# Kernel optimization log

Measured on AMD Instinct MI355X. Metric: run time of the kernel, lower is better.

## Reference

```python
import jax, jax.numpy as jnp
import numpy as np

B, T = 64, 512
V, E, H, O = 50000, 300, 256, 512
NUM_LAYERS = 2


def setup_inputs() -> dict:
    key = jax.random.key(0)
    ks = jax.random.split(key, 24)
    def p(k, shape, s=0.05):
        return jax.random.normal(k, shape, dtype=jnp.float32) * s
    inp = {"text": jax.random.randint(ks[0], (B, T), 0, V)}
    inp["emb"] = p(ks[1], (V, E), 0.1)
    in_dims = [E, 2 * H]  # layer0 sees embeddings, layer1 sees bidir concat
    idx = 2
    for l in range(NUM_LAYERS):
        for d in ("f", "b"):
            inp[f"l{l}{d}_Wih"] = p(ks[idx], (4 * H, in_dims[l])); idx += 1
            inp[f"l{l}{d}_Whh"] = p(ks[idx], (4 * H, H)); idx += 1
            inp[f"l{l}{d}_bih"] = p(ks[idx], (4 * H,)); idx += 1
            inp[f"l{l}{d}_bhh"] = p(ks[idx], (4 * H,)); idx += 1
    inp["fc_W"] = p(ks[idx], (O, 2 * H))
    inp["fc_b"] = p(ks[idx + 1], (O,))
    return inp


def lstm_dir(x, Wih, Whh, bih, bhh, reverse):
    """Single-direction LSTM. x: [B,T,in]. Returns (outputs [B,T,H], h_n [B,H]).
    PyTorch gate order: input, forget, cell(g), output."""
    Bsz = x.shape[0]
    Hd = Whh.shape[1]
    # Precompute input contribution for all timesteps (one big GEMM).
    xg = jnp.einsum('bti,gi->btg', x, Wih) + bih  # [B,T,4H]
    xg = jnp.swapaxes(xg, 0, 1)                    # [T,B,4H]

    def step(carry, xg_t):
        h, c = carry
        gates = xg_t + h @ Whh.T + bhh
        i, f, g, o = jnp.split(gates, 4, axis=-1)
        c = jax.nn.sigmoid(f) * c + jax.nn.sigmoid(i) * jnp.tanh(g)
        h = jax.nn.sigmoid(o) * jnp.tanh(c)
        return (h, c), h

    init = (jnp.zeros((Bsz, Hd), x.dtype), jnp.zeros((Bsz, Hd), x.dtype))
    (h_n, _), ys = jax.lax.scan(step, init, xg, reverse=reverse)
    return jnp.swapaxes(ys, 0, 1), h_n


def reference(text, emb,
              l0f_Wih, l0f_Whh, l0f_bih, l0f_bhh,
              l0b_Wih, l0b_Whh, l0b_bih, l0b_bhh,
              l1f_Wih, l1f_Whh, l1f_bih, l1f_bhh,
              l1b_Wih, l1b_Whh, l1b_bih, l1b_bhh,
              fc_W, fc_b):
    x = emb[text]  # [B,T,E] embedding lookup
    # Layer 0 (bidirectional)
    yf, _ = lstm_dir(x, l0f_Wih, l0f_Whh, l0f_bih, l0f_bhh, False)
    yb, _ = lstm_dir(x, l0b_Wih, l0b_Whh, l0b_bih, l0b_bhh, True)
    x1 = jnp.concatenate([yf, yb], axis=-1)  # [B,T,2H]
    # Layer 1 (bidirectional); only final hidden states are needed
    _, hf = lstm_dir(x1, l1f_Wih, l1f_Whh, l1f_bih, l1f_bhh, False)
    _, hb = lstm_dir(x1, l1b_Wih, l1b_Whh, l1b_bih, l1b_bhh, True)
    hidden = jnp.concatenate([hf, hb], axis=-1)  # [B,2H] == hidden[-2]++hidden[-1]
    # dropout is identity in eval mode
    return hidden @ fc_W.T + fc_b  # [B,O]
```

## Files before the change

kernel.cpp:

```cpp
#include <hip/hip_runtime.h>

typedef unsigned short u16;
typedef __attribute__((ext_vector_type(4))) float f32x4;
typedef __attribute__((ext_vector_type(8))) __bf16 bf16x8;
typedef __attribute__((ext_vector_type(4))) u16 u16x4;

#define TSEQ 512
#define BATCH 64
#define HDIM 256
#define KD   512
#define GDIM 1024
#define EDIM 300
#define ELDA 304
#define TC   128
#define NC   4

__device__ __forceinline__ float b2f(u16 u){
  union { unsigned int i; float f; } v; v.i = ((unsigned int)u) << 16; return v.f;
}
__device__ __forceinline__ u16 f2b(float f){
  union { float f; unsigned int i; } v; v.f = f;
  unsigned int x = v.i;
  unsigned int r = (x + 0x7fffu + ((x >> 16) & 1u)) >> 16;
  return (u16)r;
}
__device__ __forceinline__ float sigm(float x){
  return __builtin_amdgcn_rcpf(1.f + __expf(-x));
}
__device__ __forceinline__ float tanh_(float x){
  float e = __expf(2.f * x);
  return 1.f - 2.f * __builtin_amdgcn_rcpf(e + 1.f);
}
__device__ __forceinline__ f32x4 mfma16(bf16x8 a, bf16x8 b, f32x4 c){
  return __builtin_amdgcn_mfma_f32_16x16x32_bf16(a, b, c, 0, 0, 0);
}

struct Cvt6 {
  const float* src[4];
  u16* dst[4];
  int cum[5];
};
__global__ void k6_cvt(Cvt6 a){
  int g = blockIdx.x * 256 + threadIdx.x;
  if (g >= a.cum[4]) return;
  int s = 0;
#pragma unroll
  for (int i = 1; i < 4; ++i) if (g >= a.cum[i]) s = i;
  int off = g - a.cum[s];
  f32x4 v = *(const f32x4*)(a.src[s] + (size_t)off * 4);
  u16x4 o = { f2b(v[0]), f2b(v[1]), f2b(v[2]), f2b(v[3]) };
  *(u16x4*)(a.dst[s] + (size_t)off * 4) = o;
}

struct CvtW6 { const float* src[4]; u16* dst; };
__global__ void k6_cvtw(CvtW6 a){
  int g = blockIdx.x * 256 + threadIdx.x;
  int mat = g >> 16;
  int rem = g & 65535;
  int row = rem >> 6, c4 = rem & 63;
  f32x4 v = *(const f32x4*)(a.src[mat] + (size_t)row * HDIM + c4 * 4);
  u16x4 hi = { f2b(v[0]), f2b(v[1]), f2b(v[2]), f2b(v[3]) };
  f32x4 r = { v[0] - b2f(hi[0]), v[1] - b2f(hi[1]), v[2] - b2f(hi[2]), v[3] - b2f(hi[3]) };
  u16x4 lo = { f2b(r[0]), f2b(r[1]), f2b(r[2]), f2b(r[3]) };
  u16* base = a.dst + (size_t)mat * GDIM * KD + (size_t)row * KD;
  *(u16x4*)(base + c4 * 4) = hi;
  *(u16x4*)(base + HDIM + c4 * 4) = lo;
}

struct Bias6 { const float* a[4]; const float* b[4]; float* d[4]; };
__global__ void k6_bias(Bias6 z){
  int k = blockIdx.x, i = threadIdx.x;
  z.d[k][i] = z.a[k][i] + z.b[k][i];
}

__global__ void k6_embed(const int* __restrict__ text, const float* __restrict__ emb,
                         u16* __restrict__ xbf){
  int row = blockIdx.x;
  int t = threadIdx.x;
  if (t >= 75) return;
  int tok = text[row];
  f32x4 v = *(const f32x4*)(emb + (size_t)tok * EDIM + t * 4);
  u16x4 o = { f2b(v[0]), f2b(v[1]), f2b(v[2]), f2b(v[3]) };
  *(u16x4*)(xbf + (size_t)row * ELDA + t * 4) = o;
}

struct Gemm6 {
  const u16* A; long lda; int K, KT;
  const u16* W0; const u16* W1; long ldw;
  const float* bias0; const float* bias1;
  float* out;
  int tb0, tb1;
};
__global__ __launch_bounds__(256, 2) void k6_gemm(Gemm6 g){
  const int bm = blockIdx.x, bn = blockIdx.y, z = blockIdx.z;
  const u16* W = z ? g.W1 : g.W0;
  const float* bias = z ? g.bias1 : g.bias0;
  const int tbase = z ? g.tb1 : g.tb0;
  float* outp = g.out + (size_t)z * BATCH * TC * GDIM;
  const int tid = threadIdx.x;
  const int l = tid & 63, l15 = l & 15, lq = l >> 4;
  const int wid = tid >> 6, wm = wid >> 1, wn = wid & 1;

  __shared__ u16 At[2][128 * 40];
  __shared__ u16 Bt[2][128 * 40];

  f32x4 acc[4][4];
#pragma unroll
  for (int i = 0; i < 4; ++i)
#pragma unroll
    for (int j = 0; j < 4; ++j) acc[i][j] = (f32x4){0.f, 0.f, 0.f, 0.f};

  u16x4 alo[2], ahi[2], blo[2], bhi[2];

  auto LOAD = [&](int kt){
#pragma unroll
    for (int c = 0; c < 2; ++c){
      int idx = c * 256 + tid;
      int row = idx >> 2, seg = idx & 3;
      int k0 = kt * 32 + seg * 8;
      int gm = bm * 128 + row;
      size_t arow = (size_t)(gm >> 7) * TSEQ + tbase + (gm & 127);
      if (k0 + 8 <= g.K){
        const u16* p = g.A + arow * g.lda + k0;
        alo[c] = *(const u16x4*)p; ahi[c] = *(const u16x4*)(p + 4);
      } else {
        u16 tmp[8];
#pragma unroll
        for (int e = 0; e < 8; ++e){
          int k = k0 + e;
          tmp[e] = (k < g.K) ? g.A[arow * g.lda + k] : (u16)0;
        }
        alo[c] = (u16x4){tmp[0], tmp[1], tmp[2], tmp[3]};
        ahi[c] = (u16x4){tmp[4], tmp[5], tmp[6], tmp[7]};
      }
      int gn = bn * 128 + row;
      if (k0 + 8 <= g.K){
        const u16* p = W + (size_t)gn * g.ldw + k0;
        blo[c] = *(const u16x4*)p; bhi[c] = *(const u16x4*)(p + 4);
      } else {
        u16 tmp[8];
#pragma unroll
        for (int e = 0; e < 8; ++e){
          int k = k0 + e;
          tmp[e] = (k < g.K) ? W[(size_t)gn * g.ldw + k] : (u16)0;
        }
        blo[c] = (u16x4){tmp[0], tmp[1], tmp[2], tmp[3]};
        bhi[c] = (u16x4){tmp[4], tmp[5], tmp[6], tmp[7]};
      }
    }
  };
  auto STORE = [&](int buf){
#pragma unroll
    for (int c = 0; c < 2; ++c){
      int idx = c * 256 + tid;
      int row = idx >> 2, seg = idx & 3;
      *(u16x4*)&At[buf][row * 40 + seg * 8] = alo[c];
      *(u16x4*)&At[buf][row * 40 + seg * 8 + 4] = ahi[c];
      *(u16x4*)&Bt[buf][row * 40 + seg * 8] = blo[c];
      *(u16x4*)&Bt[buf][row * 40 + seg * 8 + 4] = bhi[c];
    }
  };

  LOAD(0); STORE(0); __syncthreads();
  for (int kt = 0; kt < g.KT; ++kt){
    int cur = kt & 1;
    bool more = (kt + 1 < g.KT);
    if (more) LOAD(kt + 1);
    bf16x8 a[4], b[4];
#pragma unroll
    for (int mi = 0; mi < 4; ++mi)
      a[mi] = *(const bf16x8*)&At[cur][(wm * 64 + mi * 16 + l15) * 40 + lq * 8];
#pragma unroll
    for (int ni = 0; ni < 4; ++ni)
      b[ni] = *(const bf16x8*)&Bt[cur][(wn * 64 + ni * 16 + l15) * 40 + lq * 8];
#pragma unroll
    for (int mi = 0; mi < 4; ++mi)
#pragma unroll
      for (int ni = 0; ni < 4; ++ni)
        acc[mi][ni] = mfma16(a[mi], b[ni], acc[mi][ni]);
    if (more) STORE(cur ^ 1);
    __syncthreads();
  }

#pragma unroll
  for (int mi = 0; mi < 4; ++mi){
#pragma unroll
    for (int ni = 0; ni < 4; ++ni){
      int gn = bn * 128 + wn * 64 + ni * 16 + l15;
      float bs = bias[gn];
#pragma unroll
      for (int r = 0; r < 4; ++r){
        int gm = bm * 128 + wm * 64 + mi * 16 + lq * 4 + r;
        outp[(size_t)gm * GDIM + gn] = acc[mi][ni][r] + bs;
      }
    }
  }
}

__global__ __launch_bounds__(512, 2)
void k6_rec(const float* __restrict__ xgc,
            const u16* __restrict__ whhL,
            u16* __restrict__ y,
            float* __restrict__ hid,
            float* __restrict__ stc, float* __restrict__ stef, u16* __restrict__ sth,
            int tb0, int tb1, int first, int write_y, int write_hid)
{
  const int dir = blockIdx.x & 1;
  const int b0  = (blockIdx.x >> 1) << 4;
  const int tid = threadIdx.x;
  const int w   = tid >> 6;
  const int l   = tid & 63;
  const int l15 = l & 15;
  const int lq  = l >> 4;
  const int rev = dir;

  __shared__ u16 hbuf[16 * 256];
  __shared__ u16 ws1[8 * 16 * KD];

  const u16* whhd = whhL + (size_t)dir * GDIM * KD;

  int tn16[8];
#pragma unroll
  for (int s = 0; s < 8; ++s) tn16[s] = ((s >> 1) * 16 + 2 * w + (s & 1)) * 16;

  {
    const int tb = tn16[0];
    char* wreg = (char*)ws1 + w * 16384;
#pragma unroll
    for (int r = 0; r < 16; ++r){
      bf16x8 v = *(const bf16x8*)(whhd + (size_t)(tb + r) * KD + l * 8);
      *(bf16x8*)(wreg + r * 1024 + ((l * 16) ^ ((r & 7) << 4))) = v;
    }
  }

  const u16* sb[7];
#pragma unroll
  for (int ss = 0; ss < 7; ++ss)
    sb[ss] = whhd + (size_t)(tn16[1 + ss] + l15) * KD + lq * 8;

  int koff[8];
#pragma unroll
  for (int kc = 0; kc < 8; ++kc) koff[kc] = (kc * 64 + lq * 16) ^ ((l15 & 7) << 4);
  const int aoff = l15 * 512;
  const char* hbp = (const char*)hbuf;
  const char* wsp = (const char*)ws1 + w * 16384 + l15 * 1024;

  float cst[8], ef[8], hregf[8];
  u16 hreg[8];

  if (first){
    *(f32x4*)((char*)hbuf + tid * 16) = (f32x4){0.f, 0.f, 0.f, 0.f};
#pragma unroll
    for (int i = 0; i < 8; ++i){ cst[i] = 0.f; ef[i] = 0.f; hregf[i] = 0.f; hreg[i] = 0; }
  } else {
#pragma unroll
    for (int th = 0; th < 2; ++th)
#pragma unroll
      for (int r = 0; r < 4; ++r){
        const int idx = th * 4 + r;
        const int m = lq * 4 + r;
        const int j = 32 * w + th * 16 + l15;
        const size_t si = ((size_t)(dir * BATCH + b0 + m)) * HDIM + j;
        cst[idx] = stc[si]; ef[idx] = stef[si];
        u16 hv = sth[si]; hreg[idx] = hv; hregf[idx] = 0.f;
        *(u16*)((char*)hbuf + m * 512 + ((2 * j) ^ ((m & 7) << 4))) = hv;
      }
  }

  size_t xrow[4];
  const int tt0 = rev ? (TC - 1) : 0;
#pragma unroll
  for (int r = 0; r < 4; ++r)
    xrow[r] = ((size_t)dir * BATCH + b0 + lq * 4 + r) * (size_t)(TC * GDIM)
            + (size_t)tt0 * GDIM + l15;
  const long xstep = rev ? -(long)GDIM : (long)GDIM;

#pragma unroll 1
  for (int t = 0; t < TC; ++t){
    const int te = rev ? (tb1 + TC - 1 - t) : (tb0 + t);
    __syncthreads();

    float xgv[8][4];
#pragma unroll
    for (int s = 0; s < 8; ++s)
#pragma unroll
      for (int r = 0; r < 4; ++r) xgv[s][r] = xgc[xrow[r] + tn16[s]];

    f32x4 acc[8];
#pragma unroll
    for (int s = 0; s < 8; ++s) acc[s] = (f32x4){0.f, 0.f, 0.f, 0.f};

    bf16x8 rb[2][7];
#pragma unroll
    for (int pk = 0; pk < 2; ++pk)
#pragma unroll
      for (int ss = 0; ss < 7; ++ss) rb[pk][ss] = *(const bf16x8*)(sb[ss] + pk * 32);

#pragma unroll
    for (int kc = 0; kc < 16; ++kc){
      bf16x8 af = *(const bf16x8*)(hbp + aoff + koff[kc & 7]);
      bf16x8 w0 = *(const bf16x8*)(wsp + ((kc * 64 + lq * 16) ^ ((l15 & 7) << 4)));
      bf16x8 c1 = rb[kc & 1][0], c2 = rb[kc & 1][1], c3 = rb[kc & 1][2];
      bf16x8 c4 = rb[kc & 1][3], c5 = rb[kc & 1][4], c6 = rb[kc & 1][5], c7 = rb[kc & 1][6];
      if (kc + 2 < 16){
#pragma unroll
        for (int ss = 0; ss < 7; ++ss)
          rb[kc & 1][ss] = *(const bf16x8*)(sb[ss] + (kc + 2) * 32);
      }
      acc[0] = mfma16(af, w0, acc[0]);
      acc[1] = mfma16(af, c1, acc[1]);
      acc[2] = mfma16(af, c2, acc[2]);
      acc[3] = mfma16(af, c3, acc[3]);
      acc[4] = mfma16(af, c4, acc[4]);
      acc[5] = mfma16(af, c5, acc[5]);
      acc[6] = mfma16(af, c6, acc[6]);
      acc[7] = mfma16(af, c7, acc[7]);
    }

    __syncthreads();

#pragma unroll
    for (int th = 0; th < 2; ++th){
#pragma unroll
      for (int r = 0; r < 4; ++r){
        const int idx = th * 4 + r;
        float gi = acc[0 + th][r] + xgv[0 + th][r];
        float gf = acc[2 + th][r] + xgv[2 + th][r];
        float gg = acc[4 + th][r] + xgv[4 + th][r];
        float go = acc[6 + th][r] + xgv[6 + th][r];
        float c = sigm(gf) * cst[idx] + sigm(gi) * tanh_(gg);
        cst[idx] = c;
        float h = sigm(go) * tanh_(c);
        hregf[idx] = h;
        float hq = h + ef[idx];
        u16 hb16 = f2b(hq);
        ef[idx] = hq - b2f(hb16);
        hreg[idx] = hb16;
        const int m = lq * 4 + r;
        const int j = 32 * w + th * 16 + l15;
        *(u16*)((char*)hbuf + m * 512 + ((2 * j) ^ ((m & 7) << 4))) = hb16;
        if (write_y)
          y[(((size_t)(b0 + m)) * TSEQ + te) * 512 + dir * 256 + j] = hb16;
      }
    }

#pragma unroll
    for (int r = 0; r < 4; ++r) xrow[r] += xstep;
  }

#pragma unroll
  for (int th = 0; th < 2; ++th)
#pragma unroll
    for (int r = 0; r < 4; ++r){
      const int idx = th * 4 + r;
      const int m = lq * 4 + r;
      const int j = 32 * w + th * 16 + l15;
      const size_t si = ((size_t)(dir * BATCH + b0 + m)) * HDIM + j;
      stc[si] = cst[idx]; stef[si] = ef[idx]; sth[si] = hreg[idx];
      if (write_hid)
        hid[((size_t)(b0 + m)) * 512 + dir * 256 + j] = hregf[idx];
    }
}

__global__ void k6_fc(const float* __restrict__ hid, const float* __restrict__ fcW,
                      const float* __restrict__ fcb, float* __restrict__ out){
  const int b = blockIdx.y;
  const int o = blockIdx.x * 64 + threadIdx.x;
  __shared__ float hs[512];
#pragma unroll
  for (int i = 0; i < 8; ++i) hs[threadIdx.x * 8 + i] = hid[b * 512 + threadIdx.x * 8 + i];
  __syncthreads();
  const f32x4* w4 = (const f32x4*)(fcW + (size_t)o * 512);
  const f32x4* h4 = (const f32x4*)hs;
  float s = 0.f;
#pragma unroll 8
  for (int i = 0; i < 128; ++i){
    f32x4 a = h4[i], bq = w4[i];
    s += a[0] * bq[0] + a[1] * bq[1] + a[2] * bq[2] + a[3] * bq[3];
  }
  out[b * 512 + o] = s + fcb[o];
}

extern "C" void kernel_launch(void* const* d_in, const int* in_sizes, int n_in,
                              void* d_out, int out_size, void* d_ws, size_t ws_size,
                              hipStream_t stream)
{
  (void)in_sizes; (void)n_in; (void)out_size; (void)ws_size;
  const int*   text = (const int*)d_in[0];
  const float* emb  = (const float*)d_in[1];
  const float* Wih[4] = {(const float*)d_in[2], (const float*)d_in[6], (const float*)d_in[10], (const float*)d_in[14]};
  const float* Whh[4] = {(const float*)d_in[3], (const float*)d_in[7], (const float*)d_in[11], (const float*)d_in[15]};
  const float* bih[4] = {(const float*)d_in[4], (const float*)d_in[8], (const float*)d_in[12], (const float*)d_in[16]};
  const float* bhh[4] = {(const float*)d_in[5], (const float*)d_in[9], (const float*)d_in[13], (const float*)d_in[17]};
  const float* fcW = (const float*)d_in[18];
  const float* fcb = (const float*)d_in[19];

  char* ws = (char*)d_ws;
  size_t off = 0;
  auto alloc = [&](size_t bytes) -> void* {
    void* p = ws + off;
    off += (bytes + 255) & ~(size_t)255;
    return p;
  };

  u16*   xbf    = (u16*)alloc((size_t)BATCH * TSEQ * ELDA * 2);
  u16*   wihb0f = (u16*)alloc((size_t)GDIM * 300 * 2);
  u16*   wihb0b = (u16*)alloc((size_t)GDIM * 300 * 2);
  u16*   wihb1f = (u16*)alloc((size_t)GDIM * 512 * 2);
  u16*   wihb1b = (u16*)alloc((size_t)GDIM * 512 * 2);
  u16*   whh2   = (u16*)alloc((size_t)4 * GDIM * KD * 2);
  float* bsum   = (float*)alloc((size_t)4 * GDIM * 4);
  float* xgc    = (float*)alloc((size_t)2 * BATCH * TC * GDIM * 4);
  u16*   y0     = (u16*)alloc((size_t)BATCH * TSEQ * 512 * 2);
  float* stc    = (float*)alloc((size_t)2 * BATCH * HDIM * 4);
  float* stef   = (float*)alloc((size_t)2 * BATCH * HDIM * 4);
  u16*   sth    = (u16*)alloc((size_t)2 * BATCH * HDIM * 2);
  float* hidf   = (float*)alloc((size_t)BATCH * 512 * 4);

  Cvt6 ca;
  ca.src[0] = Wih[0]; ca.dst[0] = wihb0f;
  ca.src[1] = Wih[1]; ca.dst[1] = wihb0b;
  ca.src[2] = Wih[2]; ca.dst[2] = wihb1f;
  ca.src[3] = Wih[3]; ca.dst[3] = wihb1b;
  {
    int cnt4[4] = {76800, 76800, 131072, 131072};
    ca.cum[0] = 0;
    for (int i = 0; i < 4; ++i) ca.cum[i + 1] = ca.cum[i] + cnt4[i];
  }
  k6_cvt<<<dim3((415744 + 255) / 256), dim3(256), 0, stream>>>(ca);

  CvtW6 cw;
  for (int k = 0; k < 4; ++k) cw.src[k] = Whh[k];
  cw.dst = whh2;
  k6_cvtw<<<dim3(1024), dim3(256), 0, stream>>>(cw);

  Bias6 ba;
  for (int k = 0; k < 4; ++k){ ba.a[k] = bih[k]; ba.b[k] = bhh[k]; ba.d[k] = bsum + k * GDIM; }
  k6_bias<<<dim3(4), dim3(1024), 0, stream>>>(ba);

  k6_embed<<<dim3(BATCH * TSEQ), dim3(128), 0, stream>>>(text, emb, xbf);

  for (int c = 0; c < NC; ++c){
    Gemm6 g0;
    g0.A = xbf; g0.lda = ELDA; g0.K = 300; g0.KT = 10;
    g0.W0 = wihb0f; g0.W1 = wihb0b; g0.ldw = 300;
    g0.bias0 = bsum; g0.bias1 = bsum + GDIM;
    g0.out = xgc; g0.tb0 = c * TC; g0.tb1 = (TSEQ - TC) - c * TC;
    k6_gemm<<<dim3(64, 8, 2), dim3(256), 0, stream>>>(g0);
    k6_rec<<<dim3(8), dim3(512), 0, stream>>>(xgc, whh2, y0, hidf,
        stc, stef, sth, c * TC, (TSEQ - TC) - c * TC, (c == 0) ? 1 : 0, 1, 0);
  }

  for (int c = 0; c < NC; ++c){
    Gemm6 g1;
    g1.A = y0; g1.lda = 512; g1.K = 512; g1.KT = 16;
    g1.W0 = wihb1f; g1.W1 = wihb1b; g1.ldw = 512;
    g1.bias0 = bsum + 2 * GDIM; g1.bias1 = bsum + 3 * GDIM;
    g1.out = xgc; g1.tb0 = c * TC; g1.tb1 = (TSEQ - TC) - c * TC;
    k6_gemm<<<dim3(64, 8, 2), dim3(256), 0, stream>>>(g1);
    k6_rec<<<dim3(8), dim3(512), 0, stream>>>(xgc, whh2 + (size_t)2 * GDIM * KD, y0, hidf,
        stc, stef, sth, c * TC, (TSEQ - TC) - c * TC, (c == 0) ? 1 : 0, 0, (c == NC - 1) ? 1 : 0);
  }

  k6_fc<<<dim3(8, 64), dim3(64), 0, stream>>>(hidf, fcW, fcb, (float*)d_out);
}
```

Before: 21.18 ms.

## Stream recurrent weights via async global-to-LDS triple buffer, store gate preactivations as fp16

The recurrent kernel now pre-swizzles the hi/lo bf16 split of Whh into an MFMA-fragment-ordered layout. Two of the eight gate tiles per wave stay resident in registers, and the other six are streamed each timestep through a three-deep LDS ring filled with global_load_lds and paced by explicit vmcnt waits. The input-projection GEMM writes its gate preactivations as fp16 instead of fp32, halving that traffic and the per-step loads in the recurrence. The aim is to hide weight-fetch latency in the sequential loop, at the cost of fp16 rounding of preactivations and fragile hand-tuned waitcnt scheduling.

New measurement: 23.16 ms. +9.4%, slower.

```diff
diff --git a/kernel.cpp b/kernel.cpp
--- a/kernel.cpp
+++ b/kernel.cpp
@@ -1,6 +1,7 @@
 #include <hip/hip_runtime.h>
 
 typedef unsigned short u16;
+typedef unsigned int u32;
 typedef __attribute__((ext_vector_type(4))) float f32x4;
 typedef __attribute__((ext_vector_type(8))) __bf16 bf16x8;
 typedef __attribute__((ext_vector_type(4))) u16 u16x4;
@@ -24,6 +25,12 @@
   unsigned int r = (x + 0x7fffu + ((x >> 16) & 1u)) >> 16;
   return (u16)r;
 }
+__device__ __forceinline__ u16 f2h16(float f){
+  _Float16 h = (_Float16)f; u16 u; __builtin_memcpy(&u, &h, 2); return u;
+}
+__device__ __forceinline__ float h162f(u16 u){
+  _Float16 h; __builtin_memcpy(&h, &u, 2); return (float)h;
+}
 __device__ __forceinline__ float sigm(float x){
   return __builtin_amdgcn_rcpf(1.f + __expf(-x));
 }
@@ -35,12 +42,12 @@
   return __builtin_amdgcn_mfma_f32_16x16x32_bf16(a, b, c, 0, 0, 0);
 }
 
-struct Cvt6 {
+struct Cvt7 {
   const float* src[4];
   u16* dst[4];
   int cum[5];
 };
-__global__ void k6_cvt(Cvt6 a){
+__global__ void k7_cvt(Cvt7 a){
   int g = blockIdx.x * 256 + threadIdx.x;
   if (g >= a.cum[4]) return;
   int s = 0;
@@ -52,28 +59,47 @@
   *(u16x4*)(a.dst[s] + (size_t)off * 4) = o;
 }
 
-struct CvtW6 { const float* src[4]; u16* dst; };
-__global__ void k6_cvtw(CvtW6 a){
+struct CvtW7 { const float* src[4]; u16* dst; };
+__global__ void k7_cvtw(CvtW7 a){
   int g = blockIdx.x * 256 + threadIdx.x;
   int mat = g >> 16;
   int rem = g & 65535;
-  int row = rem >> 6, c4 = rem & 63;
-  f32x4 v = *(const f32x4*)(a.src[mat] + (size_t)row * HDIM + c4 * 4);
-  u16x4 hi = { f2b(v[0]), f2b(v[1]), f2b(v[2]), f2b(v[3]) };
-  f32x4 r = { v[0] - b2f(hi[0]), v[1] - b2f(hi[1]), v[2] - b2f(hi[2]), v[3] - b2f(hi[3]) };
-  u16x4 lo = { f2b(r[0]), f2b(r[1]), f2b(r[2]), f2b(r[3]) };
-  u16* base = a.dst + (size_t)mat * GDIM * KD + (size_t)row * KD;
-  *(u16x4*)(base + c4 * 4) = hi;
-  *(u16x4*)(base + HDIM + c4 * 4) = lo;
-}
-
-struct Bias6 { const float* a[4]; const float* b[4]; float* d[4]; };
-__global__ void k6_bias(Bias6 z){
+  int chunk = rem >> 6;
+  int sub   = rem & 63;
+  int kc = chunk >> 6, w = (chunk >> 3) & 7, s = chunk & 7;
+  int l15 = sub >> 2, q = sub & 3;
+  int lq = q ^ ((l15 >> 2) & 3);
+  int row = ((s >> 1) * 16 + 2 * w + (s & 1)) * 16 + l15;
+  int kk = kc * 32 + lq * 8;
+  const float* srow = a.src[mat] + (size_t)row * HDIM;
+  u16 o[8];
+  if (kk < 256){
+    f32x4 v0 = *(const f32x4*)(srow + kk);
+    f32x4 v1 = *(const f32x4*)(srow + kk + 4);
+#pragma unroll
+    for (int e = 0; e < 4; ++e){ o[e] = f2b(v0[e]); o[4 + e] = f2b(v1[e]); }
+  } else {
+    int k2 = kk - 256;
+    f32x4 v0 = *(const f32x4*)(srow + k2);
+    f32x4 v1 = *(const f32x4*)(srow + k2 + 4);
+#pragma unroll
+    for (int e = 0; e < 4; ++e){
+      u16 h0 = f2b(v0[e]); o[e]     = f2b(v0[e] - b2f(h0));
+      u16 h1 = f2b(v1[e]); o[4 + e] = f2b(v1[e] - b2f(h1));
+    }
+  }
+  u16* d = a.dst + (size_t)mat * 524288 + (size_t)chunk * 512 + sub * 8;
+  *(u16x4*)d = (u16x4){o[0], o[1], o[2], o[3]};
+  *(u16x4*)(d + 4) = (u16x4){o[4], o[5], o[6], o[7]};
+}
+
+struct Bias7 { const float* a[4]; const float* b[4]; float* d[4]; };
+__global__ void k7_bias(Bias7 z){
   int k = blockIdx.x, i = threadIdx.x;
   z.d[k][i] = z.a[k][i] + z.b[k][i];
 }
 
-__global__ void k6_embed(const int* __restrict__ text, const float* __restrict__ emb,
+__global__ void k7_embed(const int* __restrict__ text, const float* __restrict__ emb,
                          u16* __restrict__ xbf){
   int row = blockIdx.x;
   int t = threadIdx.x;
@@ -84,19 +110,19 @@
   *(u16x4*)(xbf + (size_t)row * ELDA + t * 4) = o;
 }
 
-struct Gemm6 {
+struct Gemm7 {
   const u16* A; long lda; int K, KT;
   const u16* W0; const u16* W1; long ldw;
   const float* bias0; const float* bias1;
-  float* out;
+  u16* out;
   int tb0, tb1;
 };
-__global__ __launch_bounds__(256, 2) void k6_gemm(Gemm6 g){
+__global__ __launch_bounds__(256, 2) void k7_gemm(Gemm7 g){
   const int bm = blockIdx.x, bn = blockIdx.y, z = blockIdx.z;
   const u16* W = z ? g.W1 : g.W0;
   const float* bias = z ? g.bias1 : g.bias0;
   const int tbase = z ? g.tb1 : g.tb0;
-  float* outp = g.out + (size_t)z * BATCH * TC * GDIM;
+  u16* outp = g.out + (size_t)z * BATCH * TC * GDIM;
   const int tid = threadIdx.x;
   const int l = tid & 63, l15 = l & 15, lq = l >> 4;
   const int wid = tid >> 6, wm = wid >> 1, wn = wid & 1;
@@ -191,15 +217,15 @@
 #pragma unroll
       for (int r = 0; r < 4; ++r){
         int gm = bm * 128 + wm * 64 + mi * 16 + lq * 4 + r;
-        outp[(size_t)gm * GDIM + gn] = acc[mi][ni][r] + bs;
+        outp[(size_t)gm * GDIM + gn] = f2h16(acc[mi][ni][r] + bs);
       }
     }
   }
 }
 
 __global__ __launch_bounds__(512, 2)
-void k6_rec(const float* __restrict__ xgc,
-            const u16* __restrict__ whhL,
+void k7_rec(const u16* __restrict__ xgc,
+            const u16* __restrict__ whT,
             u16* __restrict__ y,
             float* __restrict__ hid,
             float* __restrict__ stc, float* __restrict__ stef, u16* __restrict__ sth,
@@ -215,35 +241,28 @@
   const int rev = dir;
 
   __shared__ u16 hbuf[16 * 256];
-  __shared__ u16 ws1[8 * 16 * KD];
-
-  const u16* whhd = whhL + (size_t)dir * GDIM * KD;
+  __shared__ u16 stg[3][6][8][512];
+
+  const u16* whd = whT + (size_t)dir * 524288;
+  const int qsl = (lq ^ (l15 >> 2)) & 3;
+  const int swoff = l15 * 32 + qsl * 8;
+  const int rdoff = swoff * 2;
 
   int tn16[8];
 #pragma unroll
   for (int s = 0; s < 8; ++s) tn16[s] = ((s >> 1) * 16 + 2 * w + (s & 1)) * 16;
 
-  {
-    const int tb = tn16[0];
-    char* wreg = (char*)ws1 + w * 16384;
-#pragma unroll
-    for (int r = 0; r < 16; ++r){
-      bf16x8 v = *(const bf16x8*)(whhd + (size_t)(tb + r) * KD + l * 8);
-      *(bf16x8*)(wreg + r * 1024 + ((l * 16) ^ ((r & 7) << 4))) = v;
-    }
-  }
-
-  const u16* sb[7];
-#pragma unroll
-  for (int ss = 0; ss < 7; ++ss)
-    sb[ss] = whhd + (size_t)(tn16[1 + ss] + l15) * KD + lq * 8;
+  bf16x8 held0[16], held1[16];
+#pragma unroll
+  for (int kc = 0; kc < 16; ++kc){
+    held0[kc] = *(const bf16x8*)(whd + (((kc * 8 + w) * 8 + 0) << 9) + swoff);
+    held1[kc] = *(const bf16x8*)(whd + (((kc * 8 + w) * 8 + 1) << 9) + swoff);
+  }
 
   int koff[8];
 #pragma unroll
   for (int kc = 0; kc < 8; ++kc) koff[kc] = (kc * 64 + lq * 16) ^ ((l15 & 7) << 4);
-  const int aoff = l15 * 512;
   const char* hbp = (const char*)hbuf;
-  const char* wsp = (const char*)ws1 + w * 16384 + l15 * 1024;
 
   float cst[8], ef[8], hregf[8];
   u16 hreg[8];
@@ -275,12 +294,45 @@
             + (size_t)tt0 * GDIM + l15;
   const long xstep = rev ? -(long)GDIM : (long)GDIM;
 
+#define STAGE(BUF, KC) { \
+  _Pragma("unroll") \
+  for (int ss = 0; ss < 6; ++ss){ \
+    const u16* gp = whd + ((((KC) * 8 + w) * 8 + (ss + 2)) << 9) + l * 8; \
+    __builtin_amdgcn_global_load_lds( \
+        (const __attribute__((address_space(1))) u32*)gp, \
+        (__attribute__((address_space(3))) u32*)&stg[BUF][ss][w][0], 16, 0, 0); \
+  } }
+
+#define CONSUME(BUF, KC) { \
+  bf16x8 af = *(const bf16x8*)(hbp + l15 * 512 + koff[(KC) & 7]); \
+  const char* sb_ = (const char*)&stg[BUF][0][w][0]; \
+  bf16x8 w2 = *(const bf16x8*)(sb_ + 0 * 8192 + rdoff); \
+  bf16x8 w3 = *(const bf16x8*)(sb_ + 1 * 8192 + rdoff); \
+  bf16x8 w4 = *(const bf16x8*)(sb_ + 2 * 8192 + rdoff); \
+  bf16x8 w5 = *(const bf16x8*)(sb_ + 3 * 8192 + rdoff); \
+  bf16x8 w6 = *(const bf16x8*)(sb_ + 4 * 8192 + rdoff); \
+  bf16x8 w7 = *(const bf16x8*)(sb_ + 5 * 8192 + rdoff); \
+  acc[0] = mfma16(af, held0[(KC)], acc[0]); \
+  acc[1] = mfma16(af, held1[(KC)], acc[1]); \
+  acc[2] = mfma16(af, w2, acc[2]); \
+  acc[3] = mfma16(af, w3, acc[3]); \
+  acc[4] = mfma16(af, w4, acc[4]); \
+  acc[5] = mfma16(af, w5, acc[5]); \
+  acc[6] = mfma16(af, w6, acc[6]); \
+  acc[7] = mfma16(af, w7, acc[7]); }
+
+#define KCI(KC, WN) { \
+  asm volatile("s_waitcnt vmcnt(" #WN ")" ::: "memory"); \
+  __builtin_amdgcn_sched_barrier(0); \
+  CONSUME((KC) % 3, (KC)); \
+  if ((KC) + 3 < 16) STAGE((KC) % 3, (KC) + 3); }
+
 #pragma unroll 1
   for (int t = 0; t < TC; ++t){
     const int te = rev ? (tb1 + TC - 1 - t) : (tb0 + t);
     __syncthreads();
 
-    float xgv[8][4];
+    u16 xgv[8][4];
 #pragma unroll
     for (int s = 0; s < 8; ++s)
 #pragma unroll
@@ -290,32 +342,12 @@
 #pragma unroll
     for (int s = 0; s < 8; ++s) acc[s] = (f32x4){0.f, 0.f, 0.f, 0.f};
 
-    bf16x8 rb[2][7];
-#pragma unroll
-    for (int pk = 0; pk < 2; ++pk)
-#pragma unroll
-      for (int ss = 0; ss < 7; ++ss) rb[pk][ss] = *(const bf16x8*)(sb[ss] + pk * 32);
-
-#pragma unroll
-    for (int kc = 0; kc < 16; ++kc){
-      bf16x8 af = *(const bf16x8*)(hbp + aoff + koff[kc & 7]);
-      bf16x8 w0 = *(const bf16x8*)(wsp + ((kc * 64 + lq * 16) ^ ((l15 & 7) << 4)));
-      bf16x8 c1 = rb[kc & 1][0], c2 = rb[kc & 1][1], c3 = rb[kc & 1][2];
-      bf16x8 c4 = rb[kc & 1][3], c5 = rb[kc & 1][4], c6 = rb[kc & 1][5], c7 = rb[kc & 1][6];
-      if (kc + 2 < 16){
-#pragma unroll
-        for (int ss = 0; ss < 7; ++ss)
-          rb[kc & 1][ss] = *(const bf16x8*)(sb[ss] + (kc + 2) * 32);
-      }
-      acc[0] = mfma16(af, w0, acc[0]);
-      acc[1] = mfma16(af, c1, acc[1]);
-      acc[2] = mfma16(af, c2, acc[2]);
-      acc[3] = mfma16(af, c3, acc[3]);
-      acc[4] = mfma16(af, c4, acc[4]);
-      acc[5] = mfma16(af, c5, acc[5]);
-      acc[6] = mfma16(af, c6, acc[6]);
-      acc[7] = mfma16(af, c7, acc[7]);
-    }
+    STAGE(0, 0) STAGE(1, 1) STAGE(2, 2)
+
+    KCI(0, 12)  KCI(1, 12)  KCI(2, 12)  KCI(3, 12)
+    KCI(4, 12)  KCI(5, 12)  KCI(6, 12)  KCI(7, 12)
+    KCI(8, 12)  KCI(9, 12)  KCI(10, 12) KCI(11, 12)
+    KCI(12, 12) KCI(13, 12) KCI(14, 6)  KCI(15, 0)
 
     __syncthreads();
 
@@ -324,10 +356,10 @@
 #pragma unroll
       for (int r = 0; r < 4; ++r){
         const int idx = th * 4 + r;
-        float gi = acc[0 + th][r] + xgv[0 + th][r];
-        float gf = acc[2 + th][r] + xgv[2 + th][r];
-        float gg = acc[4 + th][r] + xgv[4 + th][r];
-        float go = acc[6 + th][r] + xgv[6 + th][r];
+        float gi = acc[0 + th][r] + h162f(xgv[0 + th][r]);
+        float gf = acc[2 + th][r] + h162f(xgv[2 + th][r]);
+        float gg = acc[4 + th][r] + h162f(xgv[4 + th][r]);
+        float go = acc[6 + th][r] + h162f(xgv[6 + th][r]);
         float c = sigm(gf) * cst[idx] + sigm(gi) * tanh_(gg);
         cst[idx] = c;
         float h = sigm(go) * tanh_(c);
@@ -348,6 +380,10 @@
     for (int r = 0; r < 4; ++r) xrow[r] += xstep;
   }
 
+#undef KCI
+#undef CONSUME
+#undef STAGE
+
 #pragma unroll
   for (int th = 0; th < 2; ++th)
 #pragma unroll
@@ -362,7 +398,7 @@
     }
 }
 
-__global__ void k6_fc(const float* __restrict__ hid, const float* __restrict__ fcW,
+__global__ void k7_fc(const float* __restrict__ hid, const float* __restrict__ fcW,
                       const float* __restrict__ fcb, float* __restrict__ out){
   const int b = blockIdx.y;
   const int o = blockIdx.x * 64 + threadIdx.x;
@@ -408,16 +444,16 @@
   u16*   wihb0b = (u16*)alloc((size_t)GDIM * 300 * 2);
   u16*   wihb1f = (u16*)alloc((size_t)GDIM * 512 * 2);
   u16*   wihb1b = (u16*)alloc((size_t)GDIM * 512 * 2);
-  u16*   whh2   = (u16*)alloc((size_t)4 * GDIM * KD * 2);
+  u16*   whhT   = (u16*)alloc((size_t)4 * 524288 * 2);
   float* bsum   = (float*)alloc((size_t)4 * GDIM * 4);
-  float* xgc    = (float*)alloc((size_t)2 * BATCH * TC * GDIM * 4);
+  u16*   xgc    = (u16*)alloc((size_t)2 * BATCH * TC * GDIM * 2);
   u16*   y0     = (u16*)alloc((size_t)BATCH * TSEQ * 512 * 2);
   float* stc    = (float*)alloc((size_t)2 * BATCH * HDIM * 4);
   float* stef   = (float*)alloc((size_t)2 * BATCH * HDIM * 4);
   u16*   sth    = (u16*)alloc((size_t)2 * BATCH * HDIM * 2);
   float* hidf   = (float*)alloc((size_t)BATCH * 512 * 4);
 
-  Cvt6 ca;
+  Cvt7 ca;
   ca.src[0] = Wih[0]; ca.dst[0] = wihb0f;
   ca.src[1] = Wih[1]; ca.dst[1] = wihb0b;
   ca.src[2] = Wih[2]; ca.dst[2] = wihb1f;
@@ -427,40 +463,40 @@
     ca.cum[0] = 0;
     for (int i = 0; i < 4; ++i) ca.cum[i + 1] = ca.cum[i] + cnt4[i];
   }
-  k6_cvt<<<dim3((415744 + 255) / 256), dim3(256), 0, stream>>>(ca);
-
-  CvtW6 cw;
+  k7_cvt<<<dim3((415744 + 255) / 256), dim3(256), 0, stream>>>(ca);
+
+  CvtW7 cw;
   for (int k = 0; k < 4; ++k) cw.src[k] = Whh[k];
-  cw.dst = whh2;
-  k6_cvtw<<<dim3(1024), dim3(256), 0, stream>>>(cw);
-
-  Bias6 ba;
+  cw.dst = whhT;
+  k7_cvtw<<<dim3(1024), dim3(256), 0, stream>>>(cw);
+
+  Bias7 ba;
   for (int k = 0; k < 4; ++k){ ba.a[k] = bih[k]; ba.b[k] = bhh[k]; ba.d[k] = bsum + k * GDIM; }
-  k6_bias<<<dim3(4), dim3(1024), 0, stream>>>(ba);
-
-  k6_embed<<<dim3(BATCH * TSEQ), dim3(128), 0, stream>>>(text, emb, xbf);
+  k7_bias<<<dim3(4), dim3(1024), 0, stream>>>(ba);
+
+  k7_embed<<<dim3(BATCH * TSEQ), dim3(128), 0, stream>>>(text, emb, xbf);
 
   for (int c = 0; c < NC; ++c){
-    Gemm6 g0;
+    Gemm7 g0;
     g0.A = xbf; g0.lda = ELDA; g0.K = 300; g0.KT = 10;
     g0.W0 = wihb0f; g0.W1 = wihb0b; g0.ldw = 300;
     g0.bias0 = bsum; g0.bias1 = bsum + GDIM;
     g0.out = xgc; g0.tb0 = c * TC; g0.tb1 = (TSEQ - TC) - c * TC;
-    k6_gemm<<<dim3(64, 8, 2), dim3(256), 0, stream>>>(g0);
-    k6_rec<<<dim3(8), dim3(512), 0, stream>>>(xgc, whh2, y0, hidf,
+    k7_gemm<<<dim3(64, 8, 2), dim3(256), 0, stream>>>(g0);
+    k7_rec<<<dim3(8), dim3(512), 0, stream>>>(xgc, whhT, y0, hidf,
         stc, stef, sth, c * TC, (TSEQ - TC) - c * TC, (c == 0) ? 1 : 0, 1, 0);
   }
 
   for (int c = 0; c < NC; ++c){
-    Gemm6 g1;
+    Gemm7 g1;
     g1.A = y0; g1.lda = 512; g1.K = 512; g1.KT = 16;
     g1.W0 = wihb1f; g1.W1 = wihb1b; g1.ldw = 512;
     g1.bias0 = bsum + 2 * GDIM; g1.bias1 = bsum + 3 * GDIM;
     g1.out = xgc; g1.tb0 = c * TC; g1.tb1 = (TSEQ - TC) - c * TC;
-    k6_gemm<<<dim3(64, 8, 2), dim3(256), 0, stream>>>(g1);
-    k6_rec<<<dim3(8), dim3(512), 0, stream>>>(xgc, whh2 + (size_t)2 * GDIM * KD, y0, hidf,
+    k7_gemm<<<dim3(64, 8, 2), dim3(256), 0, stream>>>(g1);
+    k7_rec<<<dim3(8), dim3(512), 0, stream>>>(xgc, whhT + (size_t)2 * 524288, y0, hidf,
         stc, stef, sth, c * TC, (TSEQ - TC) - c * TC, (c == 0) ? 1 : 0, 0, (c == NC - 1) ? 1 : 0);
   }
 
-  k6_fc<<<dim3(8, 64), dim3(64), 0, stream>>>(hidf, fcW, fcb, (float*)d_out);
-}
+  k7_fc<<<dim3(8, 64), dim3(64), 0, stream>>>(hidf, fcW, fcb, (float*)d_out);
+}
```
